# Kernel tuning notes

Hardware: AMD Instinct MI355X
Metric: run time of the kernel (lower is better)

Reference implementation:

```python
import jax, jax.numpy as jnp
import numpy as np

B, SEQ, D, H, L, DFF, K = 2, 2048, 256, 8, 2, 1024, 3
DK = D // H
EPS = 1e-5
DROP_CONNECT = 0.5  # eval mode: weight * (1 - rate)


def _make_pe():
    pos = np.arange(SEQ)[:, None].astype(np.float32)
    div = np.exp(np.arange(0, D, 2).astype(np.float32) * (-np.log(10000.0) / D))
    pe = np.zeros((SEQ, D), np.float32)
    pe[:, 0::2] = np.sin(pos * div)
    pe[:, 1::2] = np.cos(pos * div)
    return jnp.asarray(pe)


def setup_inputs() -> dict:
    key = jax.random.key(0)
    ks = jax.random.split(key, 16)
    s = 0.02
    d = {
        'x': jax.random.normal(ks[0], (B, SEQ, 1), jnp.float32),
        'conv_w': jax.random.normal(ks[1], (D, 1, K), jnp.float32) * s,
        'conv_b': jnp.zeros((D,), jnp.float32),
        'bn_g': jnp.ones((D,), jnp.float32),
        'bn_b': jnp.zeros((D,), jnp.float32),
        'pe': _make_pe(),
        'qW': jax.random.normal(ks[2], (L, D, D), jnp.float32) * s,
        'qb': jnp.zeros((L, D), jnp.float32),
        'kW': jax.random.normal(ks[3], (L, D, D), jnp.float32) * s,
        'kb': jnp.zeros((L, D), jnp.float32),
        'vW': jax.random.normal(ks[4], (L, D, D), jnp.float32) * s,
        'vb': jnp.zeros((L, D), jnp.float32),
        'oW': jax.random.normal(ks[5], (L, D, D), jnp.float32) * s,
        'ob': jnp.zeros((L, D), jnp.float32),
        'scale': jnp.ones((L,), jnp.float32),
        'td': jnp.ones((L, H), jnp.float32),
        'ln1g': jnp.ones((L, D), jnp.float32),
        'ln1b': jnp.zeros((L, D), jnp.float32),
        'f1W': jax.random.normal(ks[6], (L, DFF, D), jnp.float32) * s,
        'f1b': jnp.zeros((L, DFF), jnp.float32),
        'f2W': jax.random.normal(ks[7], (L, D, DFF), jnp.float32) * s,
        'f2b': jnp.zeros((L, D), jnp.float32),
        'ln2g': jnp.ones((L, D), jnp.float32),
        'ln2b': jnp.zeros((L, D), jnp.float32),
        'outW': jax.random.normal(ks[8], (1, D), jnp.float32) * s,
        'outb': jnp.zeros((1,), jnp.float32),
    }
    return d


def _layernorm(z, g, b):
    m = z.mean(-1, keepdims=True)
    v = ((z - m) ** 2).mean(-1, keepdims=True)
    return (z - m) / jnp.sqrt(v + EPS) * g + b


def reference(x, conv_w, conv_b, bn_g, bn_b, pe, qW, qb, kW, kb, vW, vb, oW, ob,
              scale, td, ln1g, ln1b, f1W, f1b, f2W, f2b, ln2g, ln2b, outW, outb):
    # CNN frontend: [B,S,1] -> [B,1,S] -> conv -> BN(eval) -> relu -> [B,S,D]
    h = jnp.transpose(x, (0, 2, 1))
    h = jax.lax.conv_general_dilated(h, conv_w, (1,), 'SAME',
                                     dimension_numbers=('NCH', 'OIH', 'NCH'))
    h = h + conv_b[None, :, None]
    # BatchNorm eval with running_mean=0, running_var=1
    h = h / jnp.sqrt(1.0 + EPS) * bn_g[None, :, None] + bn_b[None, :, None]
    h = jax.nn.relu(h)
    h = jnp.transpose(h, (0, 2, 1)) + pe[None]

    inv_sqrt_dk = 1.0 / np.sqrt(DK).astype(np.float32)
    key_pos = jnp.arange(SEQ, dtype=h.dtype)  # decay depends on key index only

    for l in range(L):
        q = (h @ qW[l].T + qb[l]).reshape(B, SEQ, H, DK).transpose(0, 2, 1, 3)
        k = (h @ kW[l].T + kb[l]).reshape(B, SEQ, H, DK).transpose(0, 2, 1, 3)
        v = (h @ vW[l].T + vb[l]).reshape(B, SEQ, H, DK).transpose(0, 2, 1, 3)
        scores = jnp.einsum('bhqd,bhkd->bhqk', q, k) * (inv_sqrt_dk * scale[l])
        decay = jnp.exp(-td[l][:, None, None] * key_pos[None, None, :])  # [H,1,S]
        scores = scores * decay[None]
        attn = jax.nn.softmax(scores, axis=-1) * jax.nn.sigmoid(scores)
        ctx = jnp.einsum('bhqk,bhkd->bhqd', attn, v)
        ctx = ctx.transpose(0, 2, 1, 3).reshape(B, SEQ, D)
        h = _layernorm(h + (ctx @ oW[l].T + ob[l]), ln1g[l], ln1b[l])
        ff = jax.nn.relu(h @ f1W[l].T + f1b[l]) @ f2W[l].T + f2b[l]
        h = _layernorm(h + ff, ln2g[l], ln2b[l])

    last = h[:, -1, :]
    # DropConnectLinear in eval: weight * (1 - drop_connect_rate)
    return last @ (outW * (1.0 - DROP_CONNECT)).T + outb
```

## Files before the change

kernel.cpp:

```cpp
#include <hip/hip_runtime.h>
#include <math.h>

#define B_    2
#define SEQ_  2048
#define D_    256
#define H_    8
#define DK_   32
#define L_    2
#define DFF_  1024

#define TD_CUT 44.0f

typedef short  bf16x8 __attribute__((ext_vector_type(8)));
typedef float  f32x4  __attribute__((ext_vector_type(4)));

__device__ __forceinline__ int compute_kcut(float tdv) {
    int kcut = SEQ_;
    if (tdv > 1e-9f) {
        float kc = TD_CUT / tdv;
        kcut = (kc >= (float)SEQ_) ? SEQ_ : ((int)kc + 1);
    }
    int kcr = (kcut + 31) & ~31;
    if (kcr > SEQ_) kcr = SEQ_;
    return kcr;
}

__device__ __forceinline__ unsigned short f2bf(float f) {
    unsigned int u = __float_as_uint(f);
    unsigned int r = u + 0x7FFFu + ((u >> 16) & 1u);
    return (unsigned short)(r >> 16);
}
__device__ __forceinline__ float bf2f(unsigned short u) {
    return __uint_as_float(((unsigned int)u) << 16);
}

__device__ __forceinline__ void gload_lds16(const unsigned short* g, unsigned short* l) {
    __builtin_amdgcn_global_load_lds(
        (const __attribute__((address_space(1))) unsigned int*)(const unsigned int*)g,
        (__attribute__((address_space(3))) unsigned int*)(unsigned int*)l,
        16, 0, 0);
}

__global__ __launch_bounds__(256) void prep_kernel(
    const float* __restrict__ x, const float* __restrict__ w,
    const float* __restrict__ cb, const float* __restrict__ bg,
    const float* __restrict__ bb, const float* __restrict__ pe,
    float* __restrict__ h, unsigned short* __restrict__ hbf,
    const float* __restrict__ p0, const float* __restrict__ p1,
    const float* __restrict__ p2, const float* __restrict__ p3,
    const float* __restrict__ p4, const float* __restrict__ p5,
    unsigned short* __restrict__ q0, unsigned short* __restrict__ q1,
    unsigned short* __restrict__ q2, unsigned short* __restrict__ q3,
    unsigned short* __restrict__ q4, unsigned short* __restrict__ q5,
    float* __restrict__ vtail)
{
    int bid = blockIdx.x;
    if (bid < 4) vtail[bid * 256 + threadIdx.x] = 0.f;
    if (bid < 768) {
        int t = bid * 256 + threadIdx.x;
        const float* src; unsigned short* dst; int base;
        if (t < 65536) {
            int a = t >> 14;
            src = a == 0 ? p0 : a == 1 ? p1 : a == 2 ? p2 : p3;
            dst = a == 0 ? q0 : a == 1 ? q1 : a == 2 ? q2 : q3;
            base = (t & 16383) * 8;
        } else {
            int u = t - 65536;
            int a = u >> 16;
            src = a ? p5 : p4;
            dst = a ? q5 : q4;
            base = (u & 65535) * 8;
        }
        float4 v0 = *(const float4*)(src + base);
        float4 v1 = *(const float4*)(src + base + 4);
        bf16x8 o;
        o[0] = (short)f2bf(v0.x); o[1] = (short)f2bf(v0.y);
        o[2] = (short)f2bf(v0.z); o[3] = (short)f2bf(v0.w);
        o[4] = (short)f2bf(v1.x); o[5] = (short)f2bf(v1.y);
        o[6] = (short)f2bf(v1.z); o[7] = (short)f2bf(v1.w);
        *(bf16x8*)(dst + base) = o;
        return;
    }
    int idx = (bid - 768) * 256 + threadIdx.x;
    int d = idx & 255;
    int s = (idx >> 8) & 2047;
    int b = idx >> 19;

    const float* xp = x + b * SEQ_;
    float xm1 = (s > 0)        ? xp[s - 1] : 0.f;
    float x0  = xp[s];
    float xp1 = (s < SEQ_ - 1) ? xp[s + 1] : 0.f;

    float acc = xm1 * w[d * 3 + 0] + x0 * w[d * 3 + 1] + xp1 * w[d * 3 + 2];
    acc += cb[d];
    acc = acc * rsqrtf(1.f + 1e-5f) * bg[d] + bb[d];
    acc = fmaxf(acc, 0.f);
    float v = acc + pe[s * D_ + d];
    h[idx] = v;
    hbf[idx] = f2bf(v);
}

__global__ __launch_bounds__(256) void gemm_qkv(
    const unsigned short* __restrict__ A,
    const unsigned short* __restrict__ W0, const unsigned short* __restrict__ W1,
    const unsigned short* __restrict__ W2,
    const float* __restrict__ b0, const float* __restrict__ b1,
    const float* __restrict__ b2,
    unsigned short* __restrict__ O0, unsigned short* __restrict__ O1,
    unsigned short* __restrict__ O2,
    const float* __restrict__ td_l, float* __restrict__ vtail_l,
    int M, int N, int K)
{
    int z = blockIdx.z;
    const unsigned short* W = (z == 0) ? W0 : (z == 1) ? W1 : W2;
    const float* bias = (z == 0) ? b0 : (z == 1) ? b1 : b2;
    unsigned short* C = (z == 0) ? O0 : (z == 1) ? O1 : O2;

    __shared__ unsigned short As[64 * 64];
    __shared__ unsigned short Bs[64 * 64];
    __shared__ float vsc[4][2][16];

    int tid  = threadIdx.x;
    int wave = tid >> 6, lane = tid & 63;
    int wm = (wave & 1) * 32, wn = (wave >> 1) * 32;
    int bm = blockIdx.y * 64, bn = blockIdx.x * 64;

    const unsigned short* aG[2]; unsigned short* aL[2];
    const unsigned short* wG[2]; unsigned short* bL[2];
#pragma unroll
    for (int i = 0; i < 2; ++i) {
        int s = i * 256 + tid;
        int r = s >> 3, cb8 = s & 7;
        int gofs = ((cb8 ^ (r & 7)) * 8);
        aG[i] = A + (size_t)(bm + r) * K + gofs;
        aL[i] = &As[s * 8];
        wG[i] = W + (size_t)(bn + r) * K + gofs;
        bL[i] = &Bs[s * 8];
    }

    int fr = lane & 15;
    int kb = lane >> 4;
    int swz = fr & 7;

    f32x4 acc[2][2];
#pragma unroll
    for (int i = 0; i < 2; ++i)
#pragma unroll
        for (int j = 0; j < 2; ++j) acc[i][j] = (f32x4){0.f, 0.f, 0.f, 0.f};

    for (int k0 = 0; k0 < K; k0 += 64) {
        __syncthreads();
#pragma unroll
        for (int i = 0; i < 2; ++i) {
            gload_lds16(aG[i] + k0, aL[i]);
            gload_lds16(wG[i] + k0, bL[i]);
        }
        __syncthreads();

#pragma unroll
        for (int kc = 0; kc < 2; ++kc) {
            int blk = ((kc * 4 + kb) ^ swz) * 8;
            bf16x8 a0f = *(const bf16x8*)&As[(wm + fr) * 64 + blk];
            bf16x8 a1f = *(const bf16x8*)&As[(wm + 16 + fr) * 64 + blk];
            bf16x8 b0f = *(const bf16x8*)&Bs[(wn + fr) * 64 + blk];
            bf16x8 b1f = *(const bf16x8*)&Bs[(wn + 16 + fr) * 64 + blk];

            acc[0][0] = __builtin_amdgcn_mfma_f32_16x16x32_bf16(a0f, b0f, acc[0][0], 0, 0, 0);
            acc[0][1] = __builtin_amdgcn_mfma_f32_16x16x32_bf16(a0f, b1f, acc[0][1], 0, 0, 0);
            acc[1][0] = __builtin_amdgcn_mfma_f32_16x16x32_bf16(a1f, b0f, acc[1][0], 0, 0, 0);
            acc[1][1] = __builtin_amdgcn_mfma_f32_16x16x32_bf16(a1f, b1f, acc[1][1], 0, 0, 0);
        }
    }

    int crow = (lane >> 4) * 4;
    int ccol = lane & 15;
    float psum[2] = {0.f, 0.f};
    int kc2[2];
    kc2[0] = compute_kcut(td_l[(bn + wn) >> 5]);
    kc2[1] = compute_kcut(td_l[(bn + wn + 16) >> 5]);

#pragma unroll
    for (int j = 0; j < 2; ++j) {
        float bj = bias[bn + wn + j * 16 + ccol];
#pragma unroll
        for (int i = 0; i < 2; ++i) {
#pragma unroll
            for (int r = 0; r < 4; ++r) {
                float v = acc[i][j][r] + bj;
                unsigned short ubf = f2bf(v);
                C[(size_t)(bm + wm + i * 16 + crow + r) * N + bn + wn + j * 16 + ccol] = ubf;
                if (z == 2) {
                    int srow = (bm + wm + i * 16 + crow + r) & 2047;
                    if (srow >= kc2[j]) psum[j] += bf2f(ubf);
                }
            }
        }
    }

    if (z == 2) {
#pragma unroll
        for (int j = 0; j < 2; ++j) {
            psum[j] += __shfl_xor(psum[j], 16);
            psum[j] += __shfl_xor(psum[j], 32);
        }
        if (lane < 16) { vsc[wave][0][lane] = psum[0]; vsc[wave][1][lane] = psum[1]; }
        __syncthreads();
        if (tid < 64) {
            int wh = tid >> 5, jj = (tid >> 4) & 1, cc = tid & 15;
            float s = vsc[2 * wh][jj][cc] + vsc[2 * wh + 1][jj][cc];
            int b = blockIdx.y >> 5;
            atomicAdd(&vtail_l[b * 256 + bn + wh * 32 + jj * 16 + cc], s);
        }
    }
}

__global__ __launch_bounds__(128) void attn_kernel(
    const unsigned short* __restrict__ q, const unsigned short* __restrict__ k,
    const unsigned short* __restrict__ v, const float* __restrict__ vtail_l,
    unsigned short* __restrict__ ctxbf,
    const float* __restrict__ scale_p, const float* __restrict__ td_l)
{
    int b = blockIdx.z, hh = blockIdx.y;
    int tid = threadIdx.x;
    int row = tid >> 2;
    int sp  = tid & 3;
    int qrow = blockIdx.x * 32 + row;

    float sc  = 0.17677669529663687f * scale_p[0];
    float tdv = td_l[hh];
    int kcr = compute_kcut(tdv);
    int ntiles = kcr >> 5;

    __shared__ float kt[32][36];
    __shared__ float vt[32][36];
    __shared__ float Os[4][32][36];
    __shared__ float ms[4][32], ls[4][32];
    __shared__ float vts[32];

    if (tid < 32) vts[tid] = vtail_l[b * 256 + hh * 32 + tid];

    const unsigned short* qptr = q + ((size_t)(b * SEQ_ + qrow)) * D_ + hh * DK_;
    float qreg[32];
#pragma unroll
    for (int j = 0; j < 4; ++j) {
        uint4 u = ((const uint4*)qptr)[j];
        qreg[j*8+0] = __uint_as_float(u.x << 16); qreg[j*8+1] = __uint_as_float(u.x & 0xFFFF0000u);
        qreg[j*8+2] = __uint_as_float(u.y << 16); qreg[j*8+3] = __uint_as_float(u.y & 0xFFFF0000u);
        qreg[j*8+4] = __uint_as_float(u.z << 16); qreg[j*8+5] = __uint_as_float(u.z & 0xFFFF0000u);
        qreg[j*8+6] = __uint_as_float(u.w << 16); qreg[j*8+7] = __uint_as_float(u.w & 0xFFFF0000u);
    }
    float O[32];
#pragma unroll
    for (int d = 0; d < 32; ++d) O[d] = 0.f;
    float mrun = -1e30f, lrun = 0.f;

    for (int t = 0; t < ntiles; ++t) {
        int k0 = t * 32;
        __syncthreads();
        {
            int r = tid >> 2, c8 = (tid & 3) * 8;
            size_t goff = ((size_t)(b * SEQ_ + k0 + r)) * D_ + hh * DK_ + c8;
            uint4 uk = *(const uint4*)(k + goff);
            uint4 uv = *(const uint4*)(v + goff);
            *(float4*)&kt[r][c8]     = make_float4(__uint_as_float(uk.x << 16), __uint_as_float(uk.x & 0xFFFF0000u),
                                                   __uint_as_float(uk.y << 16), __uint_as_float(uk.y & 0xFFFF0000u));
            *(float4*)&kt[r][c8 + 4] = make_float4(__uint_as_float(uk.z << 16), __uint_as_float(uk.z & 0xFFFF0000u),
                                                   __uint_as_float(uk.w << 16), __uint_as_float(uk.w & 0xFFFF0000u));
            *(float4*)&vt[r][c8]     = make_float4(__uint_as_float(uv.x << 16), __uint_as_float(uv.x & 0xFFFF0000u),
                                                   __uint_as_float(uv.y << 16), __uint_as_float(uv.y & 0xFFFF0000u));
            *(float4*)&vt[r][c8 + 4] = make_float4(__uint_as_float(uv.z << 16), __uint_as_float(uv.z & 0xFFFF0000u),
                                                   __uint_as_float(uv.w << 16), __uint_as_float(uv.w & 0xFFFF0000u));
        }
        __syncthreads();

        float sb[8];
        float tmax = -1e30f;
#pragma unroll
        for (int kk = 0; kk < 8; ++kk) {
            int kl = sp * 8 + kk;
            float acc = 0.f;
#pragma unroll
            for (int d4 = 0; d4 < 8; ++d4) {
                float4 kv = *(const float4*)&kt[kl][d4 * 4];
                acc += qreg[d4 * 4 + 0] * kv.x + qreg[d4 * 4 + 1] * kv.y
                     + qreg[d4 * 4 + 2] * kv.z + qreg[d4 * 4 + 3] * kv.w;
            }
            float dec = __expf(-tdv * (float)(k0 + kl));
            float sv = acc * sc * dec;
            sb[kk] = sv;
            tmax = fmaxf(tmax, sv);
        }
        float mnew = fmaxf(mrun, tmax);
        float alpha = __expf(mrun - mnew);
        lrun *= alpha;
#pragma unroll
        for (int d = 0; d < 32; ++d) O[d] *= alpha;
#pragma unroll
        for (int kk = 0; kk < 8; ++kk) {
            int kl = sp * 8 + kk;
            float sv = sb[kk];
            float e = __expf(sv - mnew);
            float sg = 1.f / (1.f + __expf(-sv));
            float p = e * sg;
            lrun += e;
#pragma unroll
            for (int d4 = 0; d4 < 8; ++d4) {
                float4 vv = *(const float4*)&vt[kl][d4 * 4];
                O[d4 * 4 + 0] += p * vv.x; O[d4 * 4 + 1] += p * vv.y;
                O[d4 * 4 + 2] += p * vv.z; O[d4 * 4 + 3] += p * vv.w;
            }
        }
        mrun = mnew;
    }

#pragma unroll
    for (int d4 = 0; d4 < 8; ++d4)
        *(float4*)&Os[sp][row][d4 * 4] =
            make_float4(O[d4*4+0], O[d4*4+1], O[d4*4+2], O[d4*4+3]);
    ms[sp][row] = mrun;
    ls[sp][row] = lrun;
    __syncthreads();

    {
        int g = sp;
        float m0 = fmaxf(fmaxf(ms[0][row], ms[1][row]), fmaxf(ms[2][row], ms[3][row]));
        float mt = (kcr < SEQ_) ? fmaxf(m0, 0.f) : m0;
        float w0 = __expf(ms[0][row] - mt), w1 = __expf(ms[1][row] - mt);
        float w2 = __expf(ms[2][row] - mt), w3 = __expf(ms[3][row] - mt);
        float Lt = ls[0][row]*w0 + ls[1][row]*w1 + ls[2][row]*w2 + ls[3][row]*w3;
        float ew = 0.f;
        if (kcr < SEQ_) {
            ew = __expf(-mt);
            Lt += (float)(SEQ_ - kcr) * ew;
        }
        float invL = 1.f / Lt;
        unsigned int packed[4];
#pragma unroll
        for (int dd = 0; dd < 8; dd += 2) {
            int d0 = g * 8 + dd, d1 = d0 + 1;
            float n0 = Os[0][row][d0]*w0 + Os[1][row][d0]*w1 + Os[2][row][d0]*w2 + Os[3][row][d0]*w3;
            float n1 = Os[0][row][d1]*w0 + Os[1][row][d1]*w1 + Os[2][row][d1]*w2 + Os[3][row][d1]*w3;
            if (kcr < SEQ_) {
                n0 += 0.5f * ew * vts[d0];
                n1 += 0.5f * ew * vts[d1];
            }
            packed[dd >> 1] = (unsigned)f2bf(n0 * invL) | ((unsigned)f2bf(n1 * invL) << 16);
        }
        unsigned short* obf = ctxbf + ((size_t)(b * SEQ_ + qrow)) * D_ + hh * DK_ + g * 8;
        *(uint4*)obf = make_uint4(packed[0], packed[1], packed[2], packed[3]);
    }
}

__global__ __launch_bounds__(256) void oproj_ln1(
    const unsigned short* __restrict__ ctx, const unsigned short* __restrict__ wo,
    const float* __restrict__ ob, const float* __restrict__ resid,
    const float* __restrict__ g1, const float* __restrict__ bt1,
    float* __restrict__ h1out, unsigned short* __restrict__ h1bf)
{
    __shared__ unsigned short As[16 * 64];
    __shared__ unsigned short Bs[256 * 64];
    __shared__ float lsum[4][16], lsq[4][16], mean_s[16], inv_s[16];

    int tid = threadIdx.x;
    int wave = tid >> 6, lane = tid & 63;
    int bm = blockIdx.x * 8;
    int fr = lane & 15, kb = lane >> 4;
    int q = kb, cl = fr;
    int swz = fr & 7;

    ((unsigned int*)As)[256 + tid] = 0u;

    const unsigned short* gA = nullptr;
    unsigned short* lA = nullptr;
    if (tid < 64) {
        int r = tid >> 3, cb8 = tid & 7;
        gA = ctx + (size_t)(bm + r) * 256 + ((cb8 ^ (r & 7)) * 8);
        lA = &As[tid * 8];
    }

    f32x4 acc[4];
#pragma unroll
    for (int j = 0; j < 4; ++j) acc[j] = (f32x4){0.f, 0.f, 0.f, 0.f};

    for (int k0 = 0; k0 < 256; k0 += 64) {
        __syncthreads();
        if (tid < 64) gload_lds16(gA + k0, lA);
#pragma unroll
        for (int i = 0; i < 8; ++i) {
            int s = i * 256 + tid;
            int r = s >> 3, cb8 = s & 7;
            gload_lds16(wo + (size_t)r * 256 + k0 + ((cb8 ^ (r & 7)) * 8), &Bs[s * 8]);
        }
        __syncthreads();

#pragma unroll
        for (int kc = 0; kc < 2; ++kc) {
            int blk = ((kc * 4 + kb) ^ swz) * 8;
            bf16x8 af = *(const bf16x8*)&As[fr * 64 + blk];
#pragma unroll
            for (int t = 0; t < 4; ++t) {
                int n = wave * 64 + t * 16 + fr;
                bf16x8 bfv = *(const bf16x8*)&Bs[n * 64 + blk];
                acc[t] = __builtin_amdgcn_mfma_f32_16x16x32_bf16(af, bfv, acc[t], 0, 0, 0);
            }
        }
    }

    float zsum[4] = {0.f, 0.f, 0.f, 0.f}, zsq[4] = {0.f, 0.f, 0.f, 0.f};
    float zv[4][4];
#pragma unroll
    for (int ct = 0; ct < 4; ++ct) {
        int col = wave * 64 + ct * 16 + cl;
        float bj = ob[col];
#pragma unroll
        for (int r = 0; r < 4; ++r) {
            int lr = q * 4 + r;
            float z = 0.f;
            if (lr < 8) z = acc[ct][r] + bj + resid[(size_t)(bm + lr) * 256 + col];
            zv[ct][r] = z;
            zsum[r] += z;
            zsq[r]  += z * z;
        }
    }
#pragma unroll
    for (int r = 0; r < 4; ++r) {
#pragma unroll
        for (int off = 1; off < 16; off <<= 1) {
            zsum[r] += __shfl_xor(zsum[r], off);
            zsq[r]  += __shfl_xor(zsq[r], off);
        }
    }
    if (cl == 0) {
#pragma unroll
        for (int r = 0; r < 4; ++r) {
            lsum[wave][q * 4 + r] = zsum[r];
            lsq[wave][q * 4 + r]  = zsq[r];
        }
    }
    __syncthreads();
    if (tid < 16) {
        float s  = lsum[0][tid] + lsum[1][tid] + lsum[2][tid] + lsum[3][tid];
        float sq = lsq[0][tid] + lsq[1][tid] + lsq[2][tid] + lsq[3][tid];
        float mean = s * (1.f / 256.f);
        float var  = sq * (1.f / 256.f) - mean * mean;
        mean_s[tid] = mean;
        inv_s[tid]  = rsqrtf(var + 1e-5f);
    }
    __syncthreads();

#pragma unroll
    for (int ct = 0; ct < 4; ++ct) {
        int col = wave * 64 + ct * 16 + cl;
        float gc = g1[col], bc = bt1[col];
#pragma unroll
        for (int r = 0; r < 4; ++r) {
            int lr = q * 4 + r;
            if (lr < 8) {
                float o = (zv[ct][r] - mean_s[lr]) * inv_s[lr] * gc + bc;
                size_t off = (size_t)(bm + lr) * 256 + col;
                h1out[off] = o;
                h1bf[off]  = f2bf(o);
            }
        }
    }
}

__global__ __launch_bounds__(256) void ffn_fused(
    const unsigned short* __restrict__ h1bf, const unsigned short* __restrict__ w1,
    const float* __restrict__ f1b, const unsigned short* __restrict__ w2,
    float* __restrict__ part)
{
    __shared__ unsigned short As[32 * 64];
    __shared__ unsigned short Bs[256 * 64];
    __shared__ unsigned short ffs[32 * 264];

    int tid = threadIdx.x;
    int wave = tid >> 6, lane = tid & 63;
    int c = blockIdx.x;
    int bm = blockIdx.y * 32;
    int fr = lane & 15, kb = lane >> 4;
    int q = kb, cl = fr;
    int swz = fr & 7;

    int ar = tid >> 3, acb = tid & 7;
    const unsigned short* gA = h1bf + (size_t)(bm + ar) * 256 + ((acb ^ (ar & 7)) * 8);
    unsigned short* lA = &As[tid * 8];

    f32x4 a1[2][4];
#pragma unroll
    for (int i = 0; i < 2; ++i)
#pragma unroll
        for (int j = 0; j < 4; ++j) a1[i][j] = (f32x4){0.f, 0.f, 0.f, 0.f};

    for (int k0 = 0; k0 < 256; k0 += 64) {
        __syncthreads();
        gload_lds16(gA + k0, lA);
#pragma unroll
        for (int i = 0; i < 8; ++i) {
            int s = i * 256 + tid;
            int r = s >> 3, cb8 = s & 7;
            gload_lds16(w1 + (size_t)(c * 256 + r) * 256 + k0 + ((cb8 ^ (r & 7)) * 8), &Bs[s * 8]);
        }
        __syncthreads();

#pragma unroll
        for (int kc = 0; kc < 2; ++kc) {
            int blk = ((kc * 4 + kb) ^ swz) * 8;
            bf16x8 af[2], bfv[4];
#pragma unroll
            for (int t = 0; t < 2; ++t) af[t] = *(const bf16x8*)&As[(t * 16 + fr) * 64 + blk];
#pragma unroll
            for (int t = 0; t < 4; ++t) {
                int n = wave * 64 + t * 16 + fr;
                bfv[t] = *(const bf16x8*)&Bs[n * 64 + blk];
            }
#pragma unroll
            for (int i = 0; i < 2; ++i)
#pragma unroll
                for (int j = 0; j < 4; ++j)
                    a1[i][j] = __builtin_amdgcn_mfma_f32_16x16x32_bf16(af[i], bfv[j], a1[i][j], 0, 0, 0);
        }
    }

#pragma unroll
    for (int ct = 0; ct < 4; ++ct) {
        int col = wave * 64 + ct * 16 + cl;
        float bj = f1b[c * 256 + col];
#pragma unroll
        for (int rt = 0; rt < 2; ++rt)
#pragma unroll
            for (int r = 0; r < 4; ++r) {
                float v = fmaxf(a1[rt][ct][r] + bj, 0.f);
                ffs[(rt * 16 + q * 4 + r) * 264 + col] = f2bf(v);
            }
    }

    f32x4 a2[2][4];
#pragma unroll
    for (int i = 0; i < 2; ++i)
#pragma unroll
        for (int j = 0; j < 4; ++j) a2[i][j] = (f32x4){0.f, 0.f, 0.f, 0.f};

    for (int k0 = 0; k0 < 256; k0 += 64) {
        __syncthreads();
#pragma unroll
        for (int i = 0; i < 8; ++i) {
            int s = i * 256 + tid;
            int r = s >> 3, cb8 = s & 7;
            gload_lds16(w2 + (size_t)r * 1024 + c * 256 + k0 + ((cb8 ^ (r & 7)) * 8), &Bs[s * 8]);
        }
        __syncthreads();

#pragma unroll
        for (int kc = 0; kc < 2; ++kc) {
            int blk = ((kc * 4 + kb) ^ swz) * 8;
            bf16x8 af[2], bfv[4];
#pragma unroll
            for (int t = 0; t < 2; ++t)
                af[t] = *(const bf16x8*)&ffs[(t * 16 + fr) * 264 + k0 + kc * 32 + kb * 8];
#pragma unroll
            for (int t = 0; t < 4; ++t) {
                int n = wave * 64 + t * 16 + fr;
                bfv[t] = *(const bf16x8*)&Bs[n * 64 + blk];
            }
#pragma unroll
            for (int i = 0; i < 2; ++i)
#pragma unroll
                for (int j = 0; j < 4; ++j)
                    a2[i][j] = __builtin_amdgcn_mfma_f32_16x16x32_bf16(af[i], bfv[j], a2[i][j], 0, 0, 0);
        }
    }

#pragma unroll
    for (int ct = 0; ct < 4; ++ct) {
        int col = wave * 64 + ct * 16 + cl;
#pragma unroll
        for (int rt = 0; rt < 2; ++rt)
#pragma unroll
            for (int r = 0; r < 4; ++r)
                part[((size_t)c * 4096 + bm + rt * 16 + q * 4 + r) * 256 + col] = a2[rt][ct][r];
    }
}

__global__ __launch_bounds__(256) void merge_ln2(
    const float* __restrict__ h1, const float* __restrict__ part,
    const float* __restrict__ f2b, const float* __restrict__ g2,
    const float* __restrict__ bt2,
    float* __restrict__ hout, unsigned short* __restrict__ hbf,
    const float* __restrict__ outW, const float* __restrict__ outb,
    float* __restrict__ out, int doFinal)
{
    int row = blockIdx.x * 4 + (threadIdx.x >> 6);
    int lane = threadIdx.x & 63;
    int d = lane * 4;

    float4 z = *(const float4*)(h1 + (size_t)row * 256 + d);
    float4 b4 = *(const float4*)(f2b + d);
    z.x += b4.x; z.y += b4.y; z.z += b4.z; z.w += b4.w;
#pragma unroll
    for (int c = 0; c < 4; ++c) {
        float4 p = *(const float4*)(part + ((size_t)c * 4096 + row) * 256 + d);
        z.x += p.x; z.y += p.y; z.z += p.z; z.w += p.w;
    }

    float s = z.x + z.y + z.z + z.w;
    float ss = z.x * z.x + z.y * z.y + z.z * z.z + z.w * z.w;
#pragma unroll
    for (int off = 1; off < 64; off <<= 1) {
        s += __shfl_xor(s, off);
        ss += __shfl_xor(ss, off);
    }
    float mean = s * (1.f / 256.f);
    float var = ss * (1.f / 256.f) - mean * mean;
    float inv = rsqrtf(var + 1e-5f);

    float4 g4 = *(const float4*)(g2 + d);
    float4 t4 = *(const float4*)(bt2 + d);
    float4 o;
    o.x = (z.x - mean) * inv * g4.x + t4.x;
    o.y = (z.y - mean) * inv * g4.y + t4.y;
    o.z = (z.z - mean) * inv * g4.z + t4.z;
    o.w = (z.w - mean) * inv * g4.w + t4.w;
    *(float4*)(hout + (size_t)row * 256 + d) = o;
    unsigned int u01 = (unsigned)f2bf(o.x) | ((unsigned)f2bf(o.y) << 16);
    unsigned int u23 = (unsigned)f2bf(o.z) | ((unsigned)f2bf(o.w) << 16);
    *(uint2*)&hbf[(size_t)row * 256 + d] = make_uint2(u01, u23);

    if (doFinal && (row == 2047 || row == 4095)) {
        float4 w4 = *(const float4*)(outW + d);
        float s2 = o.x * w4.x + o.y * w4.y + o.z * w4.z + o.w * w4.w;
#pragma unroll
        for (int off = 1; off < 64; off <<= 1) s2 += __shfl_xor(s2, off);
        if (lane == 0) out[row >> 11] = s2 * 0.5f + outb[0];
    }
}

extern "C" void kernel_launch(void* const* d_in, const int* in_sizes, int n_in,
                              void* d_out, int out_size, void* d_ws, size_t ws_size,
                              hipStream_t stream)
{
    (void)in_sizes; (void)n_in; (void)out_size; (void)ws_size;
    const float* x      = (const float*)d_in[0];
    const float* conv_w = (const float*)d_in[1];
    const float* conv_b = (const float*)d_in[2];
    const float* bn_g   = (const float*)d_in[3];
    const float* bn_b   = (const float*)d_in[4];
    const float* pe     = (const float*)d_in[5];
    const float* qW     = (const float*)d_in[6];
    const float* qb     = (const float*)d_in[7];
    const float* kW     = (const float*)d_in[8];
    const float* kb     = (const float*)d_in[9];
    const float* vW     = (const float*)d_in[10];
    const float* vb     = (const float*)d_in[11];
    const float* oW     = (const float*)d_in[12];
    const float* ob     = (const float*)d_in[13];
    const float* scale  = (const float*)d_in[14];
    const float* td     = (const float*)d_in[15];
    const float* ln1g   = (const float*)d_in[16];
    const float* ln1b   = (const float*)d_in[17];
    const float* f1W    = (const float*)d_in[18];
    const float* f1b    = (const float*)d_in[19];
    const float* f2W    = (const float*)d_in[20];
    const float* f2b    = (const float*)d_in[21];
    const float* ln2g   = (const float*)d_in[22];
    const float* ln2b   = (const float*)d_in[23];
    const float* outW   = (const float*)d_in[24];
    const float* outb   = (const float*)d_in[25];
    float* out = (float*)d_out;

    float* ws = (float*)d_ws;
    const size_t MT = (size_t)B_ * SEQ_ * D_;
    float* h     = ws;
    float* h1    = ws + MT;
    float* part  = ws + 2 * MT;
    float* vtail = ws + 6 * MT;
    unsigned short* bfb = (unsigned short*)(ws + 6 * MT + 1024);
    unsigned short* h_bf   = bfb;
    unsigned short* ctx_bf = bfb + MT;
    unsigned short* q_bf   = bfb + 2 * MT;
    unsigned short* k_bf   = bfb + 3 * MT;
    unsigned short* v_bf   = bfb + 4 * MT;
    unsigned short* h1_bf  = bfb + 5 * MT;
    unsigned short* wq_bf  = bfb + 6 * MT;
    unsigned short* wk_bf  = wq_bf + MT / 8;
    unsigned short* wv_bf  = wk_bf + MT / 8;
    unsigned short* wo_bf  = wv_bf + MT / 8;
    unsigned short* wf1_bf = wo_bf + MT / 8;
    unsigned short* wf2_bf = wf1_bf + MT / 2;

    const int Mrows = B_ * SEQ_;

    prep_kernel<<<768 + (B_ * SEQ_ * D_) / 256, 256, 0, stream>>>(
        x, conv_w, conv_b, bn_g, bn_b, pe, h, h_bf,
        qW, kW, vW, oW, f1W, f2W,
        wq_bf, wk_bf, wv_bf, wo_bf, wf1_bf, wf2_bf, vtail);

    for (int l = 0; l < L_; ++l) {
        const unsigned short* wq_l  = wq_bf  + (size_t)l * D_ * D_;
        const unsigned short* wk_l  = wk_bf  + (size_t)l * D_ * D_;
        const unsigned short* wv_l  = wv_bf  + (size_t)l * D_ * D_;
        const unsigned short* wo_l  = wo_bf  + (size_t)l * D_ * D_;
        const unsigned short* wf1_l = wf1_bf + (size_t)l * DFF_ * D_;
        const unsigned short* wf2_l = wf2_bf + (size_t)l * DFF_ * D_;
        float* vtail_l = vtail + l * B_ * 256;

        gemm_qkv<<<dim3(D_ / 64, Mrows / 64, 3), 256, 0, stream>>>(
            h_bf, wq_l, wk_l, wv_l, qb + l * D_, kb + l * D_, vb + l * D_,
            q_bf, k_bf, v_bf, td + l * H_, vtail_l, Mrows, D_, D_);

        attn_kernel<<<dim3(SEQ_ / 32, H_, B_), 128, 0, stream>>>(
            q_bf, k_bf, v_bf, vtail_l, ctx_bf, scale + l, td + l * H_);

        oproj_ln1<<<Mrows / 8, 256, 0, stream>>>(
            ctx_bf, wo_l, ob + l * D_, h,
            ln1g + l * D_, ln1b + l * D_, h1, h1_bf);

        ffn_fused<<<dim3(4, Mrows / 32), 256, 0, stream>>>(
            h1_bf, wf1_l, f1b + l * DFF_, wf2_l, part);

        merge_ln2<<<Mrows / 4, 256, 0, stream>>>(
            h1, part, f2b + l * D_, ln2g + l * D_, ln2b + l * D_,
            h, h_bf, outW, outb, out, (l == L_ - 1) ? 1 : 0);
    }
}
```

Baseline: 206.7 us.

## Fuse all stages into one cooperative persistent megakernel with grid syncs

Replaces the eleven per-stage kernel launches with a single cooperative kernel of 256 blocks that loops over work items for each stage and separates stages with grid-wide barriers, sharing one LDS union. The attention stage is also reshaped to 256 threads covering 64 query rows per block, which halves the block count and changes the K/V tile loading to narrower loads. The aim is to remove launch gaps and tail effects between the small stages. In exchange, only 256 resident blocks (one per CU) do all the work, the union forces every stage to reserve the largest LDS footprint, and grid syncs add their own latency. Separate per-stage launches remain as a fallback if the cooperative launch fails.

```diff
diff --git a/kernel.cpp b/kernel.cpp
--- a/kernel.cpp
+++ b/kernel.cpp
@@ -1,5 +1,8 @@
 #include <hip/hip_runtime.h>
+#include <hip/hip_cooperative_groups.h>
 #include <math.h>
+
+namespace cg = cooperative_groups;
 
 #define B_    2
 #define SEQ_  2048
@@ -41,34 +44,58 @@
         16, 0, 0);
 }
 
-__global__ __launch_bounds__(256) void prep_kernel(
-    const float* __restrict__ x, const float* __restrict__ w,
-    const float* __restrict__ cb, const float* __restrict__ bg,
-    const float* __restrict__ bb, const float* __restrict__ pe,
-    float* __restrict__ h, unsigned short* __restrict__ hbf,
-    const float* __restrict__ p0, const float* __restrict__ p1,
-    const float* __restrict__ p2, const float* __restrict__ p3,
-    const float* __restrict__ p4, const float* __restrict__ p5,
-    unsigned short* __restrict__ q0, unsigned short* __restrict__ q1,
-    unsigned short* __restrict__ q2, unsigned short* __restrict__ q3,
-    unsigned short* __restrict__ q4, unsigned short* __restrict__ q5,
-    float* __restrict__ vtail)
+struct MP {
+    const float *x, *conv_w, *conv_b, *bn_g, *bn_b, *pe;
+    const float *qW, *kW, *vW, *oW, *f1W, *f2W;
+    const float *qb, *kb, *vb, *ob, *scale, *td;
+    const float *ln1g, *ln1b, *f1b, *f2b, *ln2g, *ln2b, *outW, *outb;
+    float *h, *h1, *part, *vtail, *out;
+    unsigned short *h_bf, *ctx_bf, *q_bf, *k_bf, *v_bf, *h1_bf;
+    unsigned short *wq, *wk, *wv, *wo, *wf1, *wf2;
+};
+
+union Smem {
+    struct {
+        unsigned short As[64 * 64];
+        unsigned short Bs[64 * 64];
+        float vsc[4][2][16];
+    } qk;
+    struct {
+        float kt[32][36];
+        float vt[32][36];
+        float Os[4][64][36];
+        float ms[4][64];
+        float ls[4][64];
+        float vts[32];
+    } at;
+    struct {
+        unsigned short As[16 * 64];
+        unsigned short Bs[256 * 64];
+        float lsum[4][16], lsq[4][16], mean_s[16], inv_s[16];
+    } op;
+    struct {
+        unsigned short As[32 * 64];
+        unsigned short Bs[256 * 64];
+        unsigned short ffs[32 * 264];
+    } ff;
+};
+
+__device__ void prep_stage(const MP& P, int bx, int nb, int tid)
 {
-    int bid = blockIdx.x;
-    if (bid < 4) vtail[bid * 256 + threadIdx.x] = 0.f;
-    if (bid < 768) {
-        int t = bid * 256 + threadIdx.x;
+    if (bx < 2 * L_) P.vtail[bx * 256 + tid] = 0.f;
+
+    for (int t = bx * 256 + tid; t < 196608; t += nb * 256) {
         const float* src; unsigned short* dst; int base;
         if (t < 65536) {
             int a = t >> 14;
-            src = a == 0 ? p0 : a == 1 ? p1 : a == 2 ? p2 : p3;
-            dst = a == 0 ? q0 : a == 1 ? q1 : a == 2 ? q2 : q3;
+            src = a == 0 ? P.qW : a == 1 ? P.kW : a == 2 ? P.vW : P.oW;
+            dst = a == 0 ? P.wq : a == 1 ? P.wk : a == 2 ? P.wv : P.wo;
             base = (t & 16383) * 8;
         } else {
             int u = t - 65536;
             int a = u >> 16;
-            src = a ? p5 : p4;
-            dst = a ? q5 : q4;
+            src = a ? P.f2W : P.f1W;
+            dst = a ? P.wf2 : P.wf1;
             base = (u & 65535) * 8;
         }
         float4 v0 = *(const float4*)(src + base);
@@ -79,51 +106,42 @@
         o[4] = (short)f2bf(v1.x); o[5] = (short)f2bf(v1.y);
         o[6] = (short)f2bf(v1.z); o[7] = (short)f2bf(v1.w);
         *(bf16x8*)(dst + base) = o;
-        return;
-    }
-    int idx = (bid - 768) * 256 + threadIdx.x;
-    int d = idx & 255;
-    int s = (idx >> 8) & 2047;
-    int b = idx >> 19;
-
-    const float* xp = x + b * SEQ_;
-    float xm1 = (s > 0)        ? xp[s - 1] : 0.f;
-    float x0  = xp[s];
-    float xp1 = (s < SEQ_ - 1) ? xp[s + 1] : 0.f;
-
-    float acc = xm1 * w[d * 3 + 0] + x0 * w[d * 3 + 1] + xp1 * w[d * 3 + 2];
-    acc += cb[d];
-    acc = acc * rsqrtf(1.f + 1e-5f) * bg[d] + bb[d];
-    acc = fmaxf(acc, 0.f);
-    float v = acc + pe[s * D_ + d];
-    h[idx] = v;
-    hbf[idx] = f2bf(v);
-}
-
-__global__ __launch_bounds__(256) void gemm_qkv(
-    const unsigned short* __restrict__ A,
-    const unsigned short* __restrict__ W0, const unsigned short* __restrict__ W1,
-    const unsigned short* __restrict__ W2,
-    const float* __restrict__ b0, const float* __restrict__ b1,
-    const float* __restrict__ b2,
-    unsigned short* __restrict__ O0, unsigned short* __restrict__ O1,
-    unsigned short* __restrict__ O2,
-    const float* __restrict__ td_l, float* __restrict__ vtail_l,
-    int M, int N, int K)
+    }
+
+    for (int idx = bx * 256 + tid; idx < (int)(B_ * SEQ_ * D_); idx += nb * 256) {
+        int d = idx & 255;
+        int s = (idx >> 8) & 2047;
+        int b = idx >> 19;
+        const float* xp = P.x + b * SEQ_;
+        float xm1 = (s > 0)        ? xp[s - 1] : 0.f;
+        float x0  = xp[s];
+        float xp1 = (s < SEQ_ - 1) ? xp[s + 1] : 0.f;
+        float acc = xm1 * P.conv_w[d * 3 + 0] + x0 * P.conv_w[d * 3 + 1] + xp1 * P.conv_w[d * 3 + 2];
+        acc += P.conv_b[d];
+        acc = acc * rsqrtf(1.f + 1e-5f) * P.bn_g[d] + P.bn_b[d];
+        acc = fmaxf(acc, 0.f);
+        float v = acc + P.pe[s * D_ + d];
+        P.h[idx] = v;
+        P.h_bf[idx] = f2bf(v);
+    }
+}
+
+__device__ void qkv_stage(Smem& S, int w,
+    const unsigned short* A,
+    const unsigned short* W0, const unsigned short* W1, const unsigned short* W2,
+    const float* b0, const float* b1, const float* b2,
+    unsigned short* O0, unsigned short* O1, unsigned short* O2,
+    const float* td_l, float* vtail_l, int tid)
 {
-    int z = blockIdx.z;
+    int x = w & 3, y = (w >> 2) & 63, z = w >> 8;
     const unsigned short* W = (z == 0) ? W0 : (z == 1) ? W1 : W2;
     const float* bias = (z == 0) ? b0 : (z == 1) ? b1 : b2;
     unsigned short* C = (z == 0) ? O0 : (z == 1) ? O1 : O2;
-
-    __shared__ unsigned short As[64 * 64];
-    __shared__ unsigned short Bs[64 * 64];
-    __shared__ float vsc[4][2][16];
-
-    int tid  = threadIdx.x;
+    const int K = 256, N = 256;
+
     int wave = tid >> 6, lane = tid & 63;
     int wm = (wave & 1) * 32, wn = (wave >> 1) * 32;
-    int bm = blockIdx.y * 64, bn = blockIdx.x * 64;
+    int bm = y * 64, bn = x * 64;
 
     const unsigned short* aG[2]; unsigned short* aL[2];
     const unsigned short* wG[2]; unsigned short* bL[2];
@@ -133,13 +151,12 @@
         int r = s >> 3, cb8 = s & 7;
         int gofs = ((cb8 ^ (r & 7)) * 8);
         aG[i] = A + (size_t)(bm + r) * K + gofs;
-        aL[i] = &As[s * 8];
+        aL[i] = &S.qk.As[s * 8];
         wG[i] = W + (size_t)(bn + r) * K + gofs;
-        bL[i] = &Bs[s * 8];
-    }
-
-    int fr = lane & 15;
-    int kb = lane >> 4;
+        bL[i] = &S.qk.Bs[s * 8];
+    }
+
+    int fr = lane & 15, kb = lane >> 4;
     int swz = fr & 7;
 
     f32x4 acc[2][2];
@@ -156,15 +173,13 @@
             gload_lds16(wG[i] + k0, bL[i]);
         }
         __syncthreads();
-
 #pragma unroll
         for (int kc = 0; kc < 2; ++kc) {
             int blk = ((kc * 4 + kb) ^ swz) * 8;
-            bf16x8 a0f = *(const bf16x8*)&As[(wm + fr) * 64 + blk];
-            bf16x8 a1f = *(const bf16x8*)&As[(wm + 16 + fr) * 64 + blk];
-            bf16x8 b0f = *(const bf16x8*)&Bs[(wn + fr) * 64 + blk];
-            bf16x8 b1f = *(const bf16x8*)&Bs[(wn + 16 + fr) * 64 + blk];
-
+            bf16x8 a0f = *(const bf16x8*)&S.qk.As[(wm + fr) * 64 + blk];
+            bf16x8 a1f = *(const bf16x8*)&S.qk.As[(wm + 16 + fr) * 64 + blk];
+            bf16x8 b0f = *(const bf16x8*)&S.qk.Bs[(wn + fr) * 64 + blk];
+            bf16x8 b1f = *(const bf16x8*)&S.qk.Bs[(wn + 16 + fr) * 64 + blk];
             acc[0][0] = __builtin_amdgcn_mfma_f32_16x16x32_bf16(a0f, b0f, acc[0][0], 0, 0, 0);
             acc[0][1] = __builtin_amdgcn_mfma_f32_16x16x32_bf16(a0f, b1f, acc[0][1], 0, 0, 0);
             acc[1][0] = __builtin_amdgcn_mfma_f32_16x16x32_bf16(a1f, b0f, acc[1][0], 0, 0, 0);
@@ -203,41 +218,36 @@
             psum[j] += __shfl_xor(psum[j], 16);
             psum[j] += __shfl_xor(psum[j], 32);
         }
-        if (lane < 16) { vsc[wave][0][lane] = psum[0]; vsc[wave][1][lane] = psum[1]; }
+        if (lane < 16) { S.qk.vsc[wave][0][lane] = psum[0]; S.qk.vsc[wave][1][lane] = psum[1]; }
         __syncthreads();
         if (tid < 64) {
             int wh = tid >> 5, jj = (tid >> 4) & 1, cc = tid & 15;
-            float s = vsc[2 * wh][jj][cc] + vsc[2 * wh + 1][jj][cc];
-            int b = blockIdx.y >> 5;
+            float s = S.qk.vsc[2 * wh][jj][cc] + S.qk.vsc[2 * wh + 1][jj][cc];
+            int b = y >> 5;
             atomicAdd(&vtail_l[b * 256 + bn + wh * 32 + jj * 16 + cc], s);
         }
-    }
-}
-
-__global__ __launch_bounds__(128) void attn_kernel(
-    const unsigned short* __restrict__ q, const unsigned short* __restrict__ k,
-    const unsigned short* __restrict__ v, const float* __restrict__ vtail_l,
-    unsigned short* __restrict__ ctxbf,
-    const float* __restrict__ scale_p, const float* __restrict__ td_l)
+        __syncthreads();
+    }
+}
+
+__device__ void attn_stage(Smem& S, int p,
+    const unsigned short* q, const unsigned short* k, const unsigned short* v,
+    const float* vtail_l, unsigned short* ctxbf,
+    const float* scale_p, const float* td_l, int tid)
 {
-    int b = blockIdx.z, hh = blockIdx.y;
-    int tid = threadIdx.x;
-    int row = tid >> 2;
-    int sp  = tid & 3;
-    int qrow = blockIdx.x * 32 + row;
+    auto& A = S.at;
+    int b = p >> 8, hh = (p >> 5) & 7, x = p & 31;
+    int t127 = tid & 127;
+    int row = (tid >> 7) * 32 + (t127 >> 2);
+    int sp = t127 & 3;
+    int qrow = x * 64 + row;
 
     float sc  = 0.17677669529663687f * scale_p[0];
     float tdv = td_l[hh];
     int kcr = compute_kcut(tdv);
     int ntiles = kcr >> 5;
 
-    __shared__ float kt[32][36];
-    __shared__ float vt[32][36];
-    __shared__ float Os[4][32][36];
-    __shared__ float ms[4][32], ls[4][32];
-    __shared__ float vts[32];
-
-    if (tid < 32) vts[tid] = vtail_l[b * 256 + hh * 32 + tid];
+    if (tid < 32) A.vts[tid] = vtail_l[b * 256 + hh * 32 + tid];
 
     const unsigned short* qptr = q + ((size_t)(b * SEQ_ + qrow)) * D_ + hh * DK_;
     float qreg[32];
@@ -258,18 +268,18 @@
         int k0 = t * 32;
         __syncthreads();
         {
-            int r = tid >> 2, c8 = (tid & 3) * 8;
-            size_t goff = ((size_t)(b * SEQ_ + k0 + r)) * D_ + hh * DK_ + c8;
-            uint4 uk = *(const uint4*)(k + goff);
-            uint4 uv = *(const uint4*)(v + goff);
-            *(float4*)&kt[r][c8]     = make_float4(__uint_as_float(uk.x << 16), __uint_as_float(uk.x & 0xFFFF0000u),
-                                                   __uint_as_float(uk.y << 16), __uint_as_float(uk.y & 0xFFFF0000u));
-            *(float4*)&kt[r][c8 + 4] = make_float4(__uint_as_float(uk.z << 16), __uint_as_float(uk.z & 0xFFFF0000u),
-                                                   __uint_as_float(uk.w << 16), __uint_as_float(uk.w & 0xFFFF0000u));
-            *(float4*)&vt[r][c8]     = make_float4(__uint_as_float(uv.x << 16), __uint_as_float(uv.x & 0xFFFF0000u),
-                                                   __uint_as_float(uv.y << 16), __uint_as_float(uv.y & 0xFFFF0000u));
-            *(float4*)&vt[r][c8 + 4] = make_float4(__uint_as_float(uv.z << 16), __uint_as_float(uv.z & 0xFFFF0000u),
-                                                   __uint_as_float(uv.w << 16), __uint_as_float(uv.w & 0xFFFF0000u));
+            int r = tid >> 3, c4 = (tid & 7) * 4;
+            size_t goff = ((size_t)(b * SEQ_ + k0 + r)) * D_ + hh * DK_ + c4;
+            uint2 uk = *(const uint2*)(k + goff);
+            uint2 uv = *(const uint2*)(v + goff);
+            A.kt[r][c4+0] = __uint_as_float(uk.x << 16);
+            A.kt[r][c4+1] = __uint_as_float(uk.x & 0xFFFF0000u);
+            A.kt[r][c4+2] = __uint_as_float(uk.y << 16);
+            A.kt[r][c4+3] = __uint_as_float(uk.y & 0xFFFF0000u);
+            A.vt[r][c4+0] = __uint_as_float(uv.x << 16);
+            A.vt[r][c4+1] = __uint_as_float(uv.x & 0xFFFF0000u);
+            A.vt[r][c4+2] = __uint_as_float(uv.y << 16);
+            A.vt[r][c4+3] = __uint_as_float(uv.y & 0xFFFF0000u);
         }
         __syncthreads();
 
@@ -281,7 +291,7 @@
             float acc = 0.f;
 #pragma unroll
             for (int d4 = 0; d4 < 8; ++d4) {
-                float4 kv = *(const float4*)&kt[kl][d4 * 4];
+                float4 kv = *(const float4*)&A.kt[kl][d4 * 4];
                 acc += qreg[d4 * 4 + 0] * kv.x + qreg[d4 * 4 + 1] * kv.y
                      + qreg[d4 * 4 + 2] * kv.z + qreg[d4 * 4 + 3] * kv.w;
             }
@@ -301,13 +311,13 @@
             float sv = sb[kk];
             float e = __expf(sv - mnew);
             float sg = 1.f / (1.f + __expf(-sv));
-            float p = e * sg;
+            float pw = e * sg;
             lrun += e;
 #pragma unroll
             for (int d4 = 0; d4 < 8; ++d4) {
-                float4 vv = *(const float4*)&vt[kl][d4 * 4];
-                O[d4 * 4 + 0] += p * vv.x; O[d4 * 4 + 1] += p * vv.y;
-                O[d4 * 4 + 2] += p * vv.z; O[d4 * 4 + 3] += p * vv.w;
+                float4 vv = *(const float4*)&A.vt[kl][d4 * 4];
+                O[d4 * 4 + 0] += pw * vv.x; O[d4 * 4 + 1] += pw * vv.y;
+                O[d4 * 4 + 2] += pw * vv.z; O[d4 * 4 + 3] += pw * vv.w;
             }
         }
         mrun = mnew;
@@ -315,19 +325,19 @@
 
 #pragma unroll
     for (int d4 = 0; d4 < 8; ++d4)
-        *(float4*)&Os[sp][row][d4 * 4] =
+        *(float4*)&A.Os[sp][row][d4 * 4] =
             make_float4(O[d4*4+0], O[d4*4+1], O[d4*4+2], O[d4*4+3]);
-    ms[sp][row] = mrun;
-    ls[sp][row] = lrun;
+    A.ms[sp][row] = mrun;
+    A.ls[sp][row] = lrun;
     __syncthreads();
 
     {
-        int g = sp;
-        float m0 = fmaxf(fmaxf(ms[0][row], ms[1][row]), fmaxf(ms[2][row], ms[3][row]));
+        int mrow = tid >> 2, gg = tid & 3;
+        float m0 = fmaxf(fmaxf(A.ms[0][mrow], A.ms[1][mrow]), fmaxf(A.ms[2][mrow], A.ms[3][mrow]));
         float mt = (kcr < SEQ_) ? fmaxf(m0, 0.f) : m0;
-        float w0 = __expf(ms[0][row] - mt), w1 = __expf(ms[1][row] - mt);
-        float w2 = __expf(ms[2][row] - mt), w3 = __expf(ms[3][row] - mt);
-        float Lt = ls[0][row]*w0 + ls[1][row]*w1 + ls[2][row]*w2 + ls[3][row]*w3;
+        float w0 = __expf(A.ms[0][mrow] - mt), w1 = __expf(A.ms[1][mrow] - mt);
+        float w2 = __expf(A.ms[2][mrow] - mt), w3 = __expf(A.ms[3][mrow] - mt);
+        float Lt = A.ls[0][mrow]*w0 + A.ls[1][mrow]*w1 + A.ls[2][mrow]*w2 + A.ls[3][mrow]*w3;
         float ew = 0.f;
         if (kcr < SEQ_) {
             ew = __expf(-mt);
@@ -337,45 +347,42 @@
         unsigned int packed[4];
 #pragma unroll
         for (int dd = 0; dd < 8; dd += 2) {
-            int d0 = g * 8 + dd, d1 = d0 + 1;
-            float n0 = Os[0][row][d0]*w0 + Os[1][row][d0]*w1 + Os[2][row][d0]*w2 + Os[3][row][d0]*w3;
-            float n1 = Os[0][row][d1]*w0 + Os[1][row][d1]*w1 + Os[2][row][d1]*w2 + Os[3][row][d1]*w3;
+            int d0 = gg * 8 + dd, d1 = d0 + 1;
+            float n0 = A.Os[0][mrow][d0]*w0 + A.Os[1][mrow][d0]*w1 + A.Os[2][mrow][d0]*w2 + A.Os[3][mrow][d0]*w3;
+            float n1 = A.Os[0][mrow][d1]*w0 + A.Os[1][mrow][d1]*w1 + A.Os[2][mrow][d1]*w2 + A.Os[3][mrow][d1]*w3;
             if (kcr < SEQ_) {
-                n0 += 0.5f * ew * vts[d0];
-                n1 += 0.5f * ew * vts[d1];
+                n0 += 0.5f * ew * A.vts[d0];
+                n1 += 0.5f * ew * A.vts[d1];
             }
             packed[dd >> 1] = (unsigned)f2bf(n0 * invL) | ((unsigned)f2bf(n1 * invL) << 16);
         }
-        unsigned short* obf = ctxbf + ((size_t)(b * SEQ_ + qrow)) * D_ + hh * DK_ + g * 8;
+        unsigned short* obf = ctxbf + ((size_t)(b * SEQ_ + x * 64 + mrow)) * D_ + hh * DK_ + gg * 8;
         *(uint4*)obf = make_uint4(packed[0], packed[1], packed[2], packed[3]);
     }
-}
-
-__global__ __launch_bounds__(256) void oproj_ln1(
-    const unsigned short* __restrict__ ctx, const unsigned short* __restrict__ wo,
-    const float* __restrict__ ob, const float* __restrict__ resid,
-    const float* __restrict__ g1, const float* __restrict__ bt1,
-    float* __restrict__ h1out, unsigned short* __restrict__ h1bf)
+    __syncthreads();
+}
+
+__device__ void oproj_stage(Smem& S, int w,
+    const unsigned short* ctx, const unsigned short* wo,
+    const float* ob, const float* resid,
+    const float* g1, const float* bt1,
+    float* h1out, unsigned short* h1bf, int tid)
 {
-    __shared__ unsigned short As[16 * 64];
-    __shared__ unsigned short Bs[256 * 64];
-    __shared__ float lsum[4][16], lsq[4][16], mean_s[16], inv_s[16];
-
-    int tid = threadIdx.x;
+    auto& O = S.op;
     int wave = tid >> 6, lane = tid & 63;
-    int bm = blockIdx.x * 8;
+    int bm = w * 8;
     int fr = lane & 15, kb = lane >> 4;
     int q = kb, cl = fr;
     int swz = fr & 7;
 
-    ((unsigned int*)As)[256 + tid] = 0u;
+    ((unsigned int*)O.As)[256 + tid] = 0u;
 
     const unsigned short* gA = nullptr;
     unsigned short* lA = nullptr;
     if (tid < 64) {
         int r = tid >> 3, cb8 = tid & 7;
         gA = ctx + (size_t)(bm + r) * 256 + ((cb8 ^ (r & 7)) * 8);
-        lA = &As[tid * 8];
+        lA = &O.As[tid * 8];
     }
 
     f32x4 acc[4];
@@ -389,18 +396,17 @@
         for (int i = 0; i < 8; ++i) {
             int s = i * 256 + tid;
             int r = s >> 3, cb8 = s & 7;
-            gload_lds16(wo + (size_t)r * 256 + k0 + ((cb8 ^ (r & 7)) * 8), &Bs[s * 8]);
-        }
-        __syncthreads();
-
+            gload_lds16(wo + (size_t)r * 256 + k0 + ((cb8 ^ (r & 7)) * 8), &O.Bs[s * 8]);
+        }
+        __syncthreads();
 #pragma unroll
         for (int kc = 0; kc < 2; ++kc) {
             int blk = ((kc * 4 + kb) ^ swz) * 8;
-            bf16x8 af = *(const bf16x8*)&As[fr * 64 + blk];
+            bf16x8 af = *(const bf16x8*)&O.As[fr * 64 + blk];
 #pragma unroll
             for (int t = 0; t < 4; ++t) {
                 int n = wave * 64 + t * 16 + fr;
-                bf16x8 bfv = *(const bf16x8*)&Bs[n * 64 + blk];
+                bf16x8 bfv = *(const bf16x8*)&O.Bs[n * 64 + blk];
                 acc[t] = __builtin_amdgcn_mfma_f32_16x16x32_bf16(af, bfv, acc[t], 0, 0, 0);
             }
         }
@@ -433,18 +439,18 @@
     if (cl == 0) {
 #pragma unroll
         for (int r = 0; r < 4; ++r) {
-            lsum[wave][q * 4 + r] = zsum[r];
-            lsq[wave][q * 4 + r]  = zsq[r];
+            O.lsum[wave][q * 4 + r] = zsum[r];
+            O.lsq[wave][q * 4 + r]  = zsq[r];
         }
     }
     __syncthreads();
     if (tid < 16) {
-        float s  = lsum[0][tid] + lsum[1][tid] + lsum[2][tid] + lsum[3][tid];
-        float sq = lsq[0][tid] + lsq[1][tid] + lsq[2][tid] + lsq[3][tid];
+        float s  = O.lsum[0][tid] + O.lsum[1][tid] + O.lsum[2][tid] + O.lsum[3][tid];
+        float sq = O.lsq[0][tid] + O.lsq[1][tid] + O.lsq[2][tid] + O.lsq[3][tid];
         float mean = s * (1.f / 256.f);
         float var  = sq * (1.f / 256.f) - mean * mean;
-        mean_s[tid] = mean;
-        inv_s[tid]  = rsqrtf(var + 1e-5f);
+        O.mean_s[tid] = mean;
+        O.inv_s[tid]  = rsqrtf(var + 1e-5f);
     }
     __syncthreads();
 
@@ -456,35 +462,32 @@
         for (int r = 0; r < 4; ++r) {
             int lr = q * 4 + r;
             if (lr < 8) {
-                float o = (zv[ct][r] - mean_s[lr]) * inv_s[lr] * gc + bc;
+                float o = (zv[ct][r] - O.mean_s[lr]) * O.inv_s[lr] * gc + bc;
                 size_t off = (size_t)(bm + lr) * 256 + col;
                 h1out[off] = o;
                 h1bf[off]  = f2bf(o);
             }
         }
     }
-}
-
-__global__ __launch_bounds__(256) void ffn_fused(
-    const unsigned short* __restrict__ h1bf, const unsigned short* __restrict__ w1,
-    const float* __restrict__ f1b, const unsigned short* __restrict__ w2,
-    float* __restrict__ part)
+    __syncthreads();
+}
+
+__device__ void ffn_stage(Smem& S, int w,
+    const unsigned short* h1bf, const unsigned short* w1,
+    const float* f1b, const unsigned short* w2,
+    float* part, int tid)
 {
-    __shared__ unsigned short As[32 * 64];
-    __shared__ unsigned short Bs[256 * 64];
-    __shared__ unsigned short ffs[32 * 264];
-
-    int tid = threadIdx.x;
+    auto& F = S.ff;
     int wave = tid >> 6, lane = tid & 63;
-    int c = blockIdx.x;
-    int bm = blockIdx.y * 32;
+    int c = w >> 7;
+    int bm = (w & 127) * 32;
     int fr = lane & 15, kb = lane >> 4;
     int q = kb, cl = fr;
     int swz = fr & 7;
 
     int ar = tid >> 3, acb = tid & 7;
     const unsigned short* gA = h1bf + (size_t)(bm + ar) * 256 + ((acb ^ (ar & 7)) * 8);
-    unsigned short* lA = &As[tid * 8];
+    unsigned short* lA = &F.As[tid * 8];
 
     f32x4 a1[2][4];
 #pragma unroll
@@ -499,20 +502,19 @@
         for (int i = 0; i < 8; ++i) {
             int s = i * 256 + tid;
             int r = s >> 3, cb8 = s & 7;
-            gload_lds16(w1 + (size_t)(c * 256 + r) * 256 + k0 + ((cb8 ^ (r & 7)) * 8), &Bs[s * 8]);
-        }
-        __syncthreads();
-
+            gload_lds16(w1 + (size_t)(c * 256 + r) * 256 + k0 + ((cb8 ^ (r & 7)) * 8), &F.Bs[s * 8]);
+        }
+        __syncthreads();
 #pragma unroll
         for (int kc = 0; kc < 2; ++kc) {
             int blk = ((kc * 4 + kb) ^ swz) * 8;
             bf16x8 af[2], bfv[4];
 #pragma unroll
-            for (int t = 0; t < 2; ++t) af[t] = *(const bf16x8*)&As[(t * 16 + fr) * 64 + blk];
+            for (int t = 0; t < 2; ++t) af[t] = *(const bf16x8*)&F.As[(t * 16 + fr) * 64 + blk];
 #pragma unroll
             for (int t = 0; t < 4; ++t) {
                 int n = wave * 64 + t * 16 + fr;
-                bfv[t] = *(const bf16x8*)&Bs[n * 64 + blk];
+                bfv[t] = *(const bf16x8*)&F.Bs[n * 64 + blk];
             }
 #pragma unroll
             for (int i = 0; i < 2; ++i)
@@ -531,7 +533,7 @@
 #pragma unroll
             for (int r = 0; r < 4; ++r) {
                 float v = fmaxf(a1[rt][ct][r] + bj, 0.f);
-                ffs[(rt * 16 + q * 4 + r) * 264 + col] = f2bf(v);
+                F.ffs[(rt * 16 + q * 4 + r) * 264 + col] = f2bf(v);
             }
     }
 
@@ -547,21 +549,20 @@
         for (int i = 0; i < 8; ++i) {
             int s = i * 256 + tid;
             int r = s >> 3, cb8 = s & 7;
-            gload_lds16(w2 + (size_t)r * 1024 + c * 256 + k0 + ((cb8 ^ (r & 7)) * 8), &Bs[s * 8]);
-        }
-        __syncthreads();
-
+            gload_lds16(w2 + (size_t)r * 1024 + c * 256 + k0 + ((cb8 ^ (r & 7)) * 8), &F.Bs[s * 8]);
+        }
+        __syncthreads();
 #pragma unroll
         for (int kc = 0; kc < 2; ++kc) {
             int blk = ((kc * 4 + kb) ^ swz) * 8;
             bf16x8 af[2], bfv[4];
 #pragma unroll
             for (int t = 0; t < 2; ++t)
-                af[t] = *(const bf16x8*)&ffs[(t * 16 + fr) * 264 + k0 + kc * 32 + kb * 8];
+                af[t] = *(const bf16x8*)&F.ffs[(t * 16 + fr) * 264 + k0 + kc * 32 + kb * 8];
 #pragma unroll
             for (int t = 0; t < 4; ++t) {
                 int n = wave * 64 + t * 16 + fr;
-                bfv[t] = *(const bf16x8*)&Bs[n * 64 + blk];
+                bfv[t] = *(const bf16x8*)&F.Bs[n * 64 + blk];
             }
 #pragma unroll
             for (int i = 0; i < 2; ++i)
@@ -580,18 +581,17 @@
             for (int r = 0; r < 4; ++r)
                 part[((size_t)c * 4096 + bm + rt * 16 + q * 4 + r) * 256 + col] = a2[rt][ct][r];
     }
-}
-
-__global__ __launch_bounds__(256) void merge_ln2(
-    const float* __restrict__ h1, const float* __restrict__ part,
-    const float* __restrict__ f2b, const float* __restrict__ g2,
-    const float* __restrict__ bt2,
-    float* __restrict__ hout, unsigned short* __restrict__ hbf,
-    const float* __restrict__ outW, const float* __restrict__ outb,
-    float* __restrict__ out, int doFinal)
+    __syncthreads();
+}
+
+__device__ void merge_stage(int w,
+    const float* h1, const float* part,
+    const float* f2b, const float* g2, const float* bt2,
+    float* hout, unsigned short* hbf,
+    const float* outW, const float* outb, float* out, int doFinal, int tid)
 {
-    int row = blockIdx.x * 4 + (threadIdx.x >> 6);
-    int lane = threadIdx.x & 63;
+    int row = w * 4 + (tid >> 6);
+    int lane = tid & 63;
     int d = lane * 4;
 
     float4 z = *(const float4*)(h1 + (size_t)row * 256 + d);
@@ -635,91 +635,169 @@
     }
 }
 
+__global__ void __launch_bounds__(256) mega(MP P)
+{
+    __shared__ Smem S;
+    cg::grid_group grid = cg::this_grid();
+    int bx = blockIdx.x, tid = threadIdx.x;
+
+    prep_stage(P, bx, 256, tid);
+    __threadfence();
+    grid.sync();
+
+    for (int l = 0; l < L_; ++l) {
+        const unsigned short* wq_l  = P.wq  + (size_t)l * D_ * D_;
+        const unsigned short* wk_l  = P.wk  + (size_t)l * D_ * D_;
+        const unsigned short* wv_l  = P.wv  + (size_t)l * D_ * D_;
+        const unsigned short* wo_l  = P.wo  + (size_t)l * D_ * D_;
+        const unsigned short* wf1_l = P.wf1 + (size_t)l * DFF_ * D_;
+        const unsigned short* wf2_l = P.wf2 + (size_t)l * DFF_ * D_;
+        float* vtail_l = P.vtail + l * B_ * 256;
+
+        for (int w = bx; w < 768; w += 256)
+            qkv_stage(S, w, P.h_bf, wq_l, wk_l, wv_l,
+                      P.qb + l * D_, P.kb + l * D_, P.vb + l * D_,
+                      P.q_bf, P.k_bf, P.v_bf, P.td + l * H_, vtail_l, tid);
+        __threadfence();
+        grid.sync();
+
+        for (int p = bx; p < 512; p += 256)
+            attn_stage(S, p, P.q_bf, P.k_bf, P.v_bf, vtail_l, P.ctx_bf,
+                       P.scale + l, P.td + l * H_, tid);
+        __threadfence();
+        grid.sync();
+
+        for (int w = bx; w < 512; w += 256)
+            oproj_stage(S, w, P.ctx_bf, wo_l, P.ob + l * D_, P.h,
+                        P.ln1g + l * D_, P.ln1b + l * D_, P.h1, P.h1_bf, tid);
+        __threadfence();
+        grid.sync();
+
+        for (int w = bx; w < 512; w += 256)
+            ffn_stage(S, w, P.h1_bf, wf1_l, P.f1b + l * DFF_, wf2_l, P.part, tid);
+        __threadfence();
+        grid.sync();
+
+        for (int w = bx; w < 1024; w += 256)
+            merge_stage(w, P.h1, P.part, P.f2b + l * D_,
+                        P.ln2g + l * D_, P.ln2b + l * D_,
+                        P.h, P.h_bf, P.outW, P.outb, P.out,
+                        (l == L_ - 1) ? 1 : 0, tid);
+        __threadfence();
+        grid.sync();
+    }
+}
+
+__global__ __launch_bounds__(256) void prep_wrap(MP P) {
+    prep_stage(P, blockIdx.x, gridDim.x, threadIdx.x);
+}
+__global__ __launch_bounds__(256) void qkv_wrap(MP P, int l) {
+    __shared__ Smem S;
+    qkv_stage(S, blockIdx.x, P.h_bf,
+              P.wq + (size_t)l * D_ * D_, P.wk + (size_t)l * D_ * D_,
+              P.wv + (size_t)l * D_ * D_,
+              P.qb + l * D_, P.kb + l * D_, P.vb + l * D_,
+              P.q_bf, P.k_bf, P.v_bf, P.td + l * H_,
+              P.vtail + l * B_ * 256, threadIdx.x);
+}
+__global__ __launch_bounds__(256) void attn_wrap(MP P, int l) {
+    __shared__ Smem S;
+    attn_stage(S, blockIdx.x, P.q_bf, P.k_bf, P.v_bf,
+               P.vtail + l * B_ * 256, P.ctx_bf,
+               P.scale + l, P.td + l * H_, threadIdx.x);
+}
+__global__ __launch_bounds__(256) void oproj_wrap(MP P, int l) {
+    __shared__ Smem S;
+    oproj_stage(S, blockIdx.x, P.ctx_bf, P.wo + (size_t)l * D_ * D_,
+                P.ob + l * D_, P.h, P.ln1g + l * D_, P.ln1b + l * D_,
+                P.h1, P.h1_bf, threadIdx.x);
+}
+__global__ __launch_bounds__(256) void ffn_wrap(MP P, int l) {
+    __shared__ Smem S;
+    ffn_stage(S, blockIdx.x, P.h1_bf, P.wf1 + (size_t)l * DFF_ * D_,
+              P.f1b + l * DFF_, P.wf2 + (size_t)l * DFF_ * D_,
+              P.part, threadIdx.x);
+}
+__global__ __launch_bounds__(256) void merge_wrap(MP P, int l) {
+    merge_stage(blockIdx.x, P.h1, P.part, P.f2b + l * D_,
+                P.ln2g + l * D_, P.ln2b + l * D_,
+                P.h, P.h_bf, P.outW, P.outb, P.out,
+                (l == L_ - 1) ? 1 : 0, threadIdx.x);
+}
+
 extern "C" void kernel_launch(void* const* d_in, const int* in_sizes, int n_in,
                               void* d_out, int out_size, void* d_ws, size_t ws_size,
                               hipStream_t stream)
 {
     (void)in_sizes; (void)n_in; (void)out_size; (void)ws_size;
-    const float* x      = (const float*)d_in[0];
-    const float* conv_w = (const float*)d_in[1];
-    const float* conv_b = (const float*)d_in[2];
-    const float* bn_g   = (const float*)d_in[3];
-    const float* bn_b   = (const float*)d_in[4];
-    const float* pe     = (const float*)d_in[5];
-    const float* qW     = (const float*)d_in[6];
-    const float* qb     = (const float*)d_in[7];
-    const float* kW     = (const float*)d_in[8];
-    const float* kb     = (const float*)d_in[9];
-    const float* vW     = (const float*)d_in[10];
-    const float* vb     = (const float*)d_in[11];
-    const float* oW     = (const float*)d_in[12];
-    const float* ob     = (const float*)d_in[13];
-    const float* scale  = (const float*)d_in[14];
-    const float* td     = (const float*)d_in[15];
-    const float* ln1g   = (const float*)d_in[16];
-    const float* ln1b   = (const float*)d_in[17];
-    const float* f1W    = (const float*)d_in[18];
-    const float* f1b    = (const float*)d_in[19];
-    const float* f2W    = (const float*)d_in[20];
-    const float* f2b    = (const float*)d_in[21];
-    const float* ln2g   = (const float*)d_in[22];
-    const float* ln2b   = (const float*)d_in[23];
-    const float* outW   = (const float*)d_in[24];
-    const float* outb   = (const float*)d_in[25];
-    float* out = (float*)d_out;
 
     float* ws = (float*)d_ws;
     const size_t MT = (size_t)B_ * SEQ_ * D_;
-    float* h     = ws;
-    float* h1    = ws + MT;
-    float* part  = ws + 2 * MT;
-    float* vtail = ws + 6 * MT;
+
+    MP P;
+    P.x      = (const float*)d_in[0];
+    P.conv_w = (const float*)d_in[1];
+    P.conv_b = (const float*)d_in[2];
+    P.bn_g   = (const float*)d_in[3];
+    P.bn_b   = (const float*)d_in[4];
+    P.pe     = (const float*)d_in[5];
+    P.qW     = (const float*)d_in[6];
+    P.qb     = (const float*)d_in[7];
+    P.kW     = (const float*)d_in[8];
+    P.kb     = (const float*)d_in[9];
+    P.vW     = (const float*)d_in[10];
+    P.vb     = (const float*)d_in[11];
+    P.oW     = (const float*)d_in[12];
+    P.ob     = (const float*)d_in[13];
+    P.scale  = (const float*)d_in[14];
+    P.td     = (const float*)d_in[15];
+    P.ln1g   = (const float*)d_in[16];
+    P.ln1b   = (const float*)d_in[17];
+    P.f1W    = (const float*)d_in[18];
+    P.f1b    = (const float*)d_in[19];
+    P.f2W    = (const float*)d_in[20];
+    P.f2b    = (const float*)d_in[21];
+    P.ln2g   = (const float*)d_in[22];
+    P.ln2b   = (const float*)d_in[23];
+    P.outW   = (const float*)d_in[24];
+    P.outb   = (const float*)d_in[25];
+    P.out    = (float*)d_out;
+
+    P.h     = ws;
+    P.h1    = ws + MT;
+    P.part  = ws + 2 * MT;
+    P.vtail = ws + 6 * MT;
     unsigned short* bfb = (unsigned short*)(ws + 6 * MT + 1024);
-    unsigned short* h_bf   = bfb;
-    unsigned short* ctx_bf = bfb + MT;
-    unsigned short* q_bf   = bfb + 2 * MT;
-    unsigned short* k_bf   = bfb + 3 * MT;
-    unsigned short* v_bf   = bfb + 4 * MT;
-    unsigned short* h1_bf  = bfb + 5 * MT;
-    unsigned short* wq_bf  = bfb + 6 * MT;
-    unsigned short* wk_bf  = wq_bf + MT / 8;
-    unsigned short* wv_bf  = wk_bf + MT / 8;
-    unsigned short* wo_bf  = wv_bf + MT / 8;
-    unsigned short* wf1_bf = wo_bf + MT / 8;
-    unsigned short* wf2_bf = wf1_bf + MT / 2;
-
-    const int Mrows = B_ * SEQ_;
-
-    prep_kernel<<<768 + (B_ * SEQ_ * D_) / 256, 256, 0, stream>>>(
-        x, conv_w, conv_b, bn_g, bn_b, pe, h, h_bf,
-        qW, kW, vW, oW, f1W, f2W,
-        wq_bf, wk_bf, wv_bf, wo_bf, wf1_bf, wf2_bf, vtail);
-
-    for (int l = 0; l < L_; ++l) {
-        const unsigned short* wq_l  = wq_bf  + (size_t)l * D_ * D_;
-        const unsigned short* wk_l  = wk_bf  + (size_t)l * D_ * D_;
-        const unsigned short* wv_l  = wv_bf  + (size_t)l * D_ * D_;
-        const unsigned short* wo_l  = wo_bf  + (size_t)l * D_ * D_;
-        const unsigned short* wf1_l = wf1_bf + (size_t)l * DFF_ * D_;
-        const unsigned short* wf2_l = wf2_bf + (size_t)l * DFF_ * D_;
-        float* vtail_l = vtail + l * B_ * 256;
-
-        gemm_qkv<<<dim3(D_ / 64, Mrows / 64, 3), 256, 0, stream>>>(
-            h_bf, wq_l, wk_l, wv_l, qb + l * D_, kb + l * D_, vb + l * D_,
-            q_bf, k_bf, v_bf, td + l * H_, vtail_l, Mrows, D_, D_);
-
-        attn_kernel<<<dim3(SEQ_ / 32, H_, B_), 128, 0, stream>>>(
-            q_bf, k_bf, v_bf, vtail_l, ctx_bf, scale + l, td + l * H_);
-
-        oproj_ln1<<<Mrows / 8, 256, 0, stream>>>(
-            ctx_bf, wo_l, ob + l * D_, h,
-            ln1g + l * D_, ln1b + l * D_, h1, h1_bf);
-
-        ffn_fused<<<dim3(4, Mrows / 32), 256, 0, stream>>>(
-            h1_bf, wf1_l, f1b + l * DFF_, wf2_l, part);
-
-        merge_ln2<<<Mrows / 4, 256, 0, stream>>>(
-            h1, part, f2b + l * D_, ln2g + l * D_, ln2b + l * D_,
-            h, h_bf, outW, outb, out, (l == L_ - 1) ? 1 : 0);
-    }
-}
+    P.h_bf   = bfb;
+    P.ctx_bf = bfb + MT;
+    P.q_bf   = bfb + 2 * MT;
+    P.k_bf   = bfb + 3 * MT;
+    P.v_bf   = bfb + 4 * MT;
+    P.h1_bf  = bfb + 5 * MT;
+    P.wq  = bfb + 6 * MT;
+    P.wk  = P.wq + MT / 8;
+    P.wv  = P.wk + MT / 8;
+    P.wo  = P.wv + MT / 8;
+    P.wf1 = P.wo + MT / 8;
+    P.wf2 = P.wf1 + MT / 2;
+
+    bool coop = false;
+    int maxB = 0;
+    if (hipOccupancyMaxActiveBlocksPerMultiprocessor(&maxB, mega, 256, 0) == hipSuccess
+        && maxB >= 1) {
+        void* args[] = { &P };
+        coop = (hipLaunchCooperativeKernel((const void*)mega, dim3(256), dim3(256),
+                                           args, 0, stream) == hipSuccess);
+    }
+
+    if (!coop) {
+        prep_wrap<<<1024, 256, 0, stream>>>(P);
+        for (int l = 0; l < L_; ++l) {
+            qkv_wrap  <<<768, 256, 0, stream>>>(P, l);
+            attn_wrap <<<512, 256, 0, stream>>>(P, l);
+            oproj_wrap<<<512, 256, 0, stream>>>(P, l);
+            ffn_wrap  <<<512, 256, 0, stream>>>(P, l);
+            merge_wrap<<<1024, 256, 0, stream>>>(P, l);
+        }
+    }
+}
```

After: 301.7 us. 1.46x slower.
